# Kernel optimization log

Measured on AMD Instinct MI355X. Metric: run time of the kernel, lower is better.

The kernel has to match this reference:

```python
import jax, jax.numpy as jnp
import numpy as np

PATCH_SIZE = 9
EPS = 1e-4


def setup_inputs() -> dict:
    key = jax.random.key(0)
    k1, k2 = jax.random.split(key)
    x1 = jax.random.normal(k1, (8, 1, 256, 256), dtype=jnp.float32)
    x2 = jax.random.normal(k2, (8, 1, 256, 256), dtype=jnp.float32)
    return {"x1": x1, "x2": x2}


def _to_patches(x, p):
    # [B,1,H,W] -> [B, p*p, Ho, Wo]; channel dim holds the p*p pixels of each patch
    # (equivalent to torch unfold+rearrange up to a global permutation, which the
    #  full-sum reduction below is invariant to).
    return jax.lax.conv_general_dilated_patches(x, (p, p), (1, 1), 'VALID')


def _norm_per_patch(x, eps):
    # normalize each patch over its p*p pixels (axis=1), matching torch's
    # mean/var over dims (-1,-2) of the [B, Ho*Wo, p, p] layout, correction=0
    mu = x.mean(axis=1, keepdims=True)
    var = x.var(axis=1, keepdims=True) + eps
    return (x - mu) / jnp.sqrt(var)


def reference(x1, x2):
    p1 = _to_patches(x1, PATCH_SIZE)
    p2 = _to_patches(x2, PATCH_SIZE)
    n1 = _norm_per_patch(p1, EPS)
    n2 = _norm_per_patch(p2, EPS)
    c, h, w = n1.shape[1], n1.shape[2], n1.shape[3]
    score = (n1 * n2).sum(axis=(1, 2, 3)) / (c * h * w)
    return score
```

## Files before the change

### kernel.cpp

```cpp
#include <hip/hip_runtime.h>

#define EPSF 1e-4f
#define H    256
#define W    256
#define HO   248
#define OW   24
#define OH   16
#define CSTR 33
#define GX   11
#define GY   16
#define NBLK (GX*GY)

__global__ __launch_bounds__(128) void ncc_kernel(
    const float* __restrict__ x1, const float* __restrict__ x2,
    float* __restrict__ ws)
{
    __shared__ float C[5][OH][CSTR];
    __shared__ float warp_part[2];

    const int b  = blockIdx.z;
    const int j0 = blockIdx.x * OW;
    const int i0 = blockIdx.y * OH;
    const int tid = threadIdx.x;

    const float* p1 = x1 + (size_t)b * (H * W);
    const float* p2 = x2 + (size_t)b * (H * W);

    {
        const int c = tid & 31;
        const int g = tid >> 5;
        const int j = j0 + c;
        const bool jok = (j < W);
        const int ibase = i0 + g * 4;

        float av[12], bv[12];
        #pragma unroll
        for (int r = 0; r < 12; ++r) {
            const int i = ibase + r;
            const bool ok = jok && (i < H);
            av[r] = ok ? p1[i * W + j] : 0.0f;
            bv[r] = ok ? p2[i * W + j] : 0.0f;
        }

        float s1 = 0.0f, s2 = 0.0f, s11 = 0.0f, s22 = 0.0f, s12 = 0.0f;
        #pragma unroll
        for (int r = 0; r < 9; ++r) {
            s1 += av[r];
            s2 += bv[r];
            s11 = fmaf(av[r], av[r], s11);
            s22 = fmaf(bv[r], bv[r], s22);
            s12 = fmaf(av[r], bv[r], s12);
        }
        const int t0 = g * 4;
        C[0][t0][c] = s1;  C[1][t0][c] = s2;
        C[2][t0][c] = s11; C[3][t0][c] = s22; C[4][t0][c] = s12;

        #pragma unroll
        for (int tt = 1; tt < 4; ++tt) {
            const float an = av[tt + 8], bn = bv[tt + 8];
            const float ao = av[tt - 1], bo = bv[tt - 1];
            s1 += an - ao;
            s2 += bn - bo;
            s11 = fmaf(an, an, s11); s11 = fmaf(-ao, ao, s11);
            s22 = fmaf(bn, bn, s22); s22 = fmaf(-bo, bo, s22);
            s12 = fmaf(an, bn, s12); s12 = fmaf(-ao, bo, s12);
            const int t = t0 + tt;
            C[0][t][c] = s1;  C[1][t][c] = s2;
            C[2][t][c] = s11; C[3][t][c] = s22; C[4][t][c] = s12;
        }
    }
    __syncthreads();

    float contrib = 0.0f;
    {
        const int t   = tid & 15;
        const int jg  = tid >> 4;
        const int jc0 = jg * 3;
        const int t_out = i0 + t;

        float cv[11];
        float Wq[3][5];
        #pragma unroll
        for (int q = 0; q < 5; ++q) {
            #pragma unroll
            for (int k = 0; k < 11; ++k)
                cv[k] = C[q][t][jc0 + k];
            float w = cv[0];
            #pragma unroll
            for (int k = 1; k < 9; ++k) w += cv[k];
            Wq[0][q] = w;
            Wq[1][q] = Wq[0][q] - cv[0] + cv[9];
            Wq[2][q] = Wq[1][q] - cv[1] + cv[10];
        }

        const float inv_n = 1.0f / 81.0f;
        #pragma unroll
        for (int m = 0; m < 3; ++m) {
            const int j_out = j0 + jc0 + m;
            if (t_out < HO && j_out < HO) {
                const float s1  = Wq[m][0], s2  = Wq[m][1];
                const float s11 = Wq[m][2], s22 = Wq[m][3], s12 = Wq[m][4];
                const float mu1 = s1 * inv_n;
                const float mu2 = s2 * inv_n;
                const float v1  = fmaf(-mu1, mu1, s11 * inv_n) + EPSF;
                const float v2  = fmaf(-mu2, mu2, s22 * inv_n) + EPSF;
                const float cross = fmaf(-mu1, s2, s12);
                contrib += cross * rsqrtf(v1 * v2);
            }
        }
    }

    #pragma unroll
    for (int off = 32; off >= 1; off >>= 1)
        contrib += __shfl_down(contrib, off, 64);

    const int lane = tid & 63;
    const int wid  = tid >> 6;
    if (lane == 0) warp_part[wid] = contrib;
    __syncthreads();

    if (tid == 0) {
        const int blk = blockIdx.y * GX + blockIdx.x;
        ws[b * NBLK + blk] = warp_part[0] + warp_part[1];
    }
}

__global__ __launch_bounds__(256) void ncc_reduce_kernel(
    const float* __restrict__ ws, float* __restrict__ out)
{
    const int b   = blockIdx.x;
    const int tid = threadIdx.x;

    float v = (tid < NBLK) ? ws[b * NBLK + tid] : 0.0f;

    #pragma unroll
    for (int off = 32; off >= 1; off >>= 1)
        v += __shfl_down(v, off, 64);

    __shared__ float wp[4];
    const int lane = tid & 63;
    const int wv   = tid >> 6;
    if (lane == 0) wp[wv] = v;
    __syncthreads();

    if (tid == 0) {
        const float scale = 1.0f / (81.0f * (float)HO * (float)HO);
        out[b] = (wp[0] + wp[1] + wp[2] + wp[3]) * scale;
    }
}

extern "C" void kernel_launch(void* const* d_in, const int* in_sizes, int n_in,
                              void* d_out, int out_size, void* d_ws, size_t ws_size,
                              hipStream_t stream) {
    const float* x1 = (const float*)d_in[0];
    const float* x2 = (const float*)d_in[1];
    float* out = (float*)d_out;
    float* ws  = (float*)d_ws;

    dim3 block(128);
    dim3 grid(GX, GY, 8);
    ncc_kernel<<<grid, block, 0, stream>>>(x1, x2, ws);
    ncc_reduce_kernel<<<dim3(8), dim3(256), 0, stream>>>(ws, out);
}
```

Before: 11.33 us.

## Widen column tile to 48 and give each thread eight outputs with float4 LDS reads

Doubles the output tile width per block (GX 11→6) and has each loader thread compute eight vertical sliding sums instead of four, while each compute thread now produces eight horizontal outputs from vectorized float4 shared-memory reads. This lowers the halo reload overhead and redundant horizontal window work per output, and cuts the block count. In exchange only 112 of 128 threads load and 96 compute, registers per thread rise, and the grid gets smaller, which may lower parallelism on a large GPU. The reduce kernel is shrunk to 128 threads to match the smaller per-batch partial count.

New measurement: 11.92 us. +5.1%, slower.

```diff
diff --git a/kernel.cpp b/kernel.cpp
--- a/kernel.cpp
+++ b/kernel.cpp
@@ -4,10 +4,11 @@
 #define H    256
 #define W    256
 #define HO   248
-#define OW   24
+#define OW   48
 #define OH   16
-#define CSTR 33
-#define GX   11
+#define PC   56
+#define CSTR 60
+#define GX   6
 #define GY   16
 #define NBLK (GX*GY)
 
@@ -15,7 +16,7 @@
     const float* __restrict__ x1, const float* __restrict__ x2,
     float* __restrict__ ws)
 {
-    __shared__ float C[5][OH][CSTR];
+    __shared__ __align__(16) float C[5][OH][CSTR];
     __shared__ float warp_part[2];
 
     const int b  = blockIdx.z;
@@ -26,16 +27,16 @@
     const float* p1 = x1 + (size_t)b * (H * W);
     const float* p2 = x2 + (size_t)b * (H * W);
 
-    {
-        const int c = tid & 31;
-        const int g = tid >> 5;
+    if (tid < 112) {
+        const int c = tid % PC;
+        const int g = tid / PC;
         const int j = j0 + c;
         const bool jok = (j < W);
-        const int ibase = i0 + g * 4;
+        const int ibase = i0 + g * 8;
 
-        float av[12], bv[12];
+        float av[16], bv[16];
         #pragma unroll
-        for (int r = 0; r < 12; ++r) {
+        for (int r = 0; r < 16; ++r) {
             const int i = ibase + r;
             const bool ok = jok && (i < H);
             av[r] = ok ? p1[i * W + j] : 0.0f;
@@ -51,12 +52,12 @@
             s22 = fmaf(bv[r], bv[r], s22);
             s12 = fmaf(av[r], bv[r], s12);
         }
-        const int t0 = g * 4;
+        const int t0 = g * 8;
         C[0][t0][c] = s1;  C[1][t0][c] = s2;
         C[2][t0][c] = s11; C[3][t0][c] = s22; C[4][t0][c] = s12;
 
         #pragma unroll
-        for (int tt = 1; tt < 4; ++tt) {
+        for (int tt = 1; tt < 8; ++tt) {
             const float an = av[tt + 8], bn = bv[tt + 8];
             const float ao = av[tt - 1], bo = bv[tt - 1];
             s1 += an - ao;
@@ -72,30 +73,35 @@
     __syncthreads();
 
     float contrib = 0.0f;
-    {
-        const int t   = tid & 15;
-        const int jg  = tid >> 4;
-        const int jc0 = jg * 3;
+    if (tid < 96) {
+        const int t   = tid / 6;
+        const int jg  = tid - t * 6;
+        const int jc0 = jg * 8;
         const int t_out = i0 + t;
 
-        float cv[11];
-        float Wq[3][5];
+        float Wq[8][5];
         #pragma unroll
         for (int q = 0; q < 5; ++q) {
+            const float4* rp = reinterpret_cast<const float4*>(&C[q][t][jc0]);
+            float cv[16];
             #pragma unroll
-            for (int k = 0; k < 11; ++k)
-                cv[k] = C[q][t][jc0 + k];
+            for (int k4 = 0; k4 < 4; ++k4) {
+                const float4 v4 = rp[k4];
+                cv[k4 * 4 + 0] = v4.x; cv[k4 * 4 + 1] = v4.y;
+                cv[k4 * 4 + 2] = v4.z; cv[k4 * 4 + 3] = v4.w;
+            }
             float w = cv[0];
             #pragma unroll
             for (int k = 1; k < 9; ++k) w += cv[k];
             Wq[0][q] = w;
-            Wq[1][q] = Wq[0][q] - cv[0] + cv[9];
-            Wq[2][q] = Wq[1][q] - cv[1] + cv[10];
+            #pragma unroll
+            for (int m = 1; m < 8; ++m)
+                Wq[m][q] = Wq[m - 1][q] - cv[m - 1] + cv[m + 8];
         }
 
         const float inv_n = 1.0f / 81.0f;
         #pragma unroll
-        for (int m = 0; m < 3; ++m) {
+        for (int m = 0; m < 8; ++m) {
             const int j_out = j0 + jc0 + m;
             if (t_out < HO && j_out < HO) {
                 const float s1  = Wq[m][0], s2  = Wq[m][1];
@@ -125,7 +131,7 @@
     }
 }
 
-__global__ __launch_bounds__(256) void ncc_reduce_kernel(
+__global__ __launch_bounds__(128) void ncc_reduce_kernel(
     const float* __restrict__ ws, float* __restrict__ out)
 {
     const int b   = blockIdx.x;
@@ -137,7 +143,7 @@
     for (int off = 32; off >= 1; off >>= 1)
         v += __shfl_down(v, off, 64);
 
-    __shared__ float wp[4];
+    __shared__ float wp[2];
     const int lane = tid & 63;
     const int wv   = tid >> 6;
     if (lane == 0) wp[wv] = v;
@@ -145,7 +151,7 @@
 
     if (tid == 0) {
         const float scale = 1.0f / (81.0f * (float)HO * (float)HO);
-        out[b] = (wp[0] + wp[1] + wp[2] + wp[3]) * scale;
+        out[b] = (wp[0] + wp[1]) * scale;
     }
 }
 
@@ -160,5 +166,5 @@
     dim3 block(128);
     dim3 grid(GX, GY, 8);
     ncc_kernel<<<grid, block, 0, stream>>>(x1, x2, ws);
-    ncc_reduce_kernel<<<dim3(8), dim3(256), 0, stream>>>(ws, out);
+    ncc_reduce_kernel<<<dim3(8), dim3(128), 0, stream>>>(ws, out);
 }
```

## Fuse final reduction into main kernel via last-block atomic counter

Applied to the files above, without the earlier changes.

Removes the separate reduction kernel launch. Each block writes its partial sum, then bumps a per-batch atomic counter. The block that sees the count reach a multiple of NBLK reduces that batch's partials and writes the output. The counter is never reset, and the modulo trick keeps it correct across repeated calls, provided the workspace persists and starts at a multiple of NBLK. This saves one launch at the cost of an atomic per block and a serial tail in the winning block.

New measurement: 11.96 us. 1.06x slower.

```diff
diff --git a/kernel.cpp b/kernel.cpp
--- a/kernel.cpp
+++ b/kernel.cpp
@@ -13,10 +13,11 @@
 
 __global__ __launch_bounds__(128) void ncc_kernel(
     const float* __restrict__ x1, const float* __restrict__ x2,
-    float* __restrict__ ws)
+    float* __restrict__ ws, float* __restrict__ out)
 {
     __shared__ float C[5][OH][CSTR];
     __shared__ float warp_part[2];
+    __shared__ int   winner_flag;
 
     const int b  = blockIdx.z;
     const int j0 = blockIdx.x * OW;
@@ -121,31 +122,34 @@
 
     if (tid == 0) {
         const int blk = blockIdx.y * GX + blockIdx.x;
-        ws[b * NBLK + blk] = warp_part[0] + warp_part[1];
+        const float part = warp_part[0] + warp_part[1];
+        __hip_atomic_store(&ws[b * NBLK + blk], part,
+                           __ATOMIC_RELAXED, __HIP_MEMORY_SCOPE_AGENT);
+        asm volatile("s_waitcnt vmcnt(0)" ::: "memory");
+        unsigned* cnt = (unsigned*)ws + 4096 + b * 64;
+        const unsigned old = __hip_atomic_fetch_add(cnt, 1u,
+                           __ATOMIC_RELAXED, __HIP_MEMORY_SCOPE_AGENT);
+        winner_flag = ((old % (unsigned)NBLK) == (unsigned)(NBLK - 1)) ? 1 : 0;
     }
-}
-
-__global__ __launch_bounds__(256) void ncc_reduce_kernel(
-    const float* __restrict__ ws, float* __restrict__ out)
-{
-    const int b   = blockIdx.x;
-    const int tid = threadIdx.x;
-
-    float v = (tid < NBLK) ? ws[b * NBLK + tid] : 0.0f;
-
-    #pragma unroll
-    for (int off = 32; off >= 1; off >>= 1)
-        v += __shfl_down(v, off, 64);
-
-    __shared__ float wp[4];
-    const int lane = tid & 63;
-    const int wv   = tid >> 6;
-    if (lane == 0) wp[wv] = v;
     __syncthreads();
 
-    if (tid == 0) {
-        const float scale = 1.0f / (81.0f * (float)HO * (float)HO);
-        out[b] = (wp[0] + wp[1] + wp[2] + wp[3]) * scale;
+    if (winner_flag && tid < 64) {
+        __builtin_amdgcn_fence(__ATOMIC_ACQUIRE, "agent");
+        const float* base = ws + (size_t)b * NBLK;
+        float v = __hip_atomic_load(&base[tid], __ATOMIC_ACQUIRE,
+                                    __HIP_MEMORY_SCOPE_AGENT)
+                + __hip_atomic_load(&base[tid + 64], __ATOMIC_ACQUIRE,
+                                    __HIP_MEMORY_SCOPE_AGENT);
+        if (tid < NBLK - 128)
+            v += __hip_atomic_load(&base[tid + 128], __ATOMIC_ACQUIRE,
+                                   __HIP_MEMORY_SCOPE_AGENT);
+        #pragma unroll
+        for (int off = 32; off >= 1; off >>= 1)
+            v += __shfl_down(v, off, 64);
+        if (tid == 0) {
+            const float scale = 1.0f / (81.0f * (float)HO * (float)HO);
+            out[b] = v * scale;
+        }
     }
 }
 
@@ -159,6 +163,5 @@
 
     dim3 block(128);
     dim3 grid(GX, GY, 8);
-    ncc_kernel<<<grid, block, 0, stream>>>(x1, x2, ws);
-    ncc_reduce_kernel<<<dim3(8), dim3(256), 0, stream>>>(ws, out);
+    ncc_kernel<<<grid, block, 0, stream>>>(x1, x2, ws, out);
 }
```
